# Optimization experiments

Hardware: AMD Instinct MI355X
Metric: run time of the kernel (lower is better)

The kernel has to match this reference:

```python
import jax, jax.numpy as jnp
import numpy as np

B, S, D = 4, 2048, 2048
H = 16
Q_LORA = 1536
KV_LORA = 512
D_NOPE = 128
D_ROPE = 64
D_V = 128
MLP = 8192
EPS = 1e-6
THETA = 10000.0


def rmsnorm(x, scale, eps=EPS):
    var = jnp.mean(jnp.square(x.astype(jnp.float32)), axis=-1, keepdims=True)
    return (x * jax.lax.rsqrt(var + eps)).astype(x.dtype) * scale


def rope(x, positions):
    # x: [B, S, H, d], positions: [B, S]
    d = x.shape[-1]
    inv_freq = 1.0 / (THETA ** (jnp.arange(0, d, 2, dtype=jnp.float32) / d))
    ang = positions.astype(jnp.float32)[..., None] * inv_freq  # [B,S,d/2]
    cos = jnp.cos(ang)[:, :, None, :]
    sin = jnp.sin(ang)[:, :, None, :]
    x1, x2 = jnp.split(x, 2, axis=-1)
    return jnp.concatenate([x1 * cos - x2 * sin, x2 * cos + x1 * sin], axis=-1)


def setup_inputs() -> dict:
    key = jax.random.key(0)
    ks = jax.random.split(key, 16)
    sd = lambda fan: 1.0 / np.sqrt(fan)
    inp = {
        'inputs': jax.random.normal(ks[0], (B, S, D), jnp.float32),
        'decoder_segment_ids': jnp.ones((B, S), jnp.int32),
        'decoder_positions': jnp.broadcast_to(jnp.arange(S, dtype=jnp.int32), (B, S)),
        'pre_ln_scale': jnp.ones((D,), jnp.float32),
        'post_ln_scale': jnp.ones((D,), jnp.float32),
        'q_ln_scale': jnp.ones((Q_LORA,), jnp.float32),
        'kv_ln_scale': jnp.ones((KV_LORA,), jnp.float32),
        'wq_a': jax.random.normal(ks[1], (D, Q_LORA), jnp.float32) * sd(D),
        'wq_b': jax.random.normal(ks[2], (Q_LORA, H, D_NOPE + D_ROPE), jnp.float32) * sd(Q_LORA),
        'wkv_a': jax.random.normal(ks[3], (D, KV_LORA + D_ROPE), jnp.float32) * sd(D),
        'wkv_b': jax.random.normal(ks[4], (KV_LORA, H, D_NOPE + D_V), jnp.float32) * sd(KV_LORA),
        'wo_attn': jax.random.normal(ks[5], (H, D_V, D), jnp.float32) * sd(H * D_V),
        'wi_0': jax.random.normal(ks[6], (D, MLP), jnp.float32) * sd(D),
        'wi_1': jax.random.normal(ks[7], (D, MLP), jnp.float32) * sd(D),
        'wo_mlp': jax.random.normal(ks[8], (MLP, D), jnp.float32) * sd(MLP),
    }
    return inp


def reference(inputs, decoder_segment_ids, decoder_positions, pre_ln_scale, post_ln_scale,
              q_ln_scale, kv_ln_scale, wq_a, wq_b, wkv_a, wkv_b, wo_attn, wi_0, wi_1, wo_mlp):
    # ---- pre-norm ----
    lnx = rmsnorm(inputs, pre_ln_scale)

    # ---- MLA attention ----
    # low-rank query: down-proj, norm, up-proj
    q_c = rmsnorm(lnx @ wq_a, q_ln_scale)                       # [B,S,Q_LORA]
    q = jnp.einsum('bsr,rhd->bshd', q_c, wq_b)                  # [B,S,H,nope+rope]
    q_nope, q_rope = q[..., :D_NOPE], q[..., D_NOPE:]

    # compressed kv + decoupled rope key
    kv = lnx @ wkv_a                                            # [B,S,KV_LORA+rope]
    c_kv = rmsnorm(kv[..., :KV_LORA], kv_ln_scale)
    k_rope = kv[..., KV_LORA:][:, :, None, :]                   # [B,S,1,rope]
    kvu = jnp.einsum('bsr,rhd->bshd', c_kv, wkv_b)              # [B,S,H,nope+v]
    k_nope, v = kvu[..., :D_NOPE], kvu[..., D_NOPE:]

    q_rope = rope(q_rope, decoder_positions)
    k_rope = rope(k_rope, decoder_positions)
    k_rope = jnp.broadcast_to(k_rope, (B, S, H, D_ROPE))

    qf = jnp.concatenate([q_nope, q_rope], axis=-1)             # [B,S,H,192]
    kf = jnp.concatenate([k_nope, k_rope], axis=-1)

    scale = 1.0 / np.sqrt(D_NOPE + D_ROPE)
    scores = jnp.einsum('bqhd,bkhd->bhqk', qf, kf) * scale      # [B,H,S,S]

    pos = decoder_positions
    seg = decoder_segment_ids
    mask = (pos[:, :, None] >= pos[:, None, :]) & (seg[:, :, None] == seg[:, None, :])
    scores = jnp.where(mask[:, None, :, :], scores, -1e9)
    probs = jax.nn.softmax(scores, axis=-1)

    attn = jnp.einsum('bhqk,bkhd->bqhd', probs, v)              # [B,S,H,D_V]
    attn_out = jnp.einsum('bqhd,hdm->bqm', attn, wo_attn)       # [B,S,D]

    # ---- residual + post-norm ----
    intermediate = inputs + attn_out
    hidden = rmsnorm(intermediate, post_ln_scale)

    # ---- gated MLP (silu * linear) ----
    mlp = (jax.nn.silu(hidden @ wi_0) * (hidden @ wi_1)) @ wo_mlp

    return mlp + intermediate
```

## Files before the change

### kernel.cpp

```cpp
#include <hip/hip_runtime.h>
#include <stdint.h>

typedef unsigned short u16;
typedef __bf16 bf16x8 __attribute__((ext_vector_type(8)));
typedef float f32x4 __attribute__((ext_vector_type(4)));

#define B_ 4
#define S_ 2048
#define H_ 16
#define TOK (B_*S_)
#define MFMA_B16 __builtin_amdgcn_mfma_f32_16x16x32_bf16

__device__ __forceinline__ u16 f32_bf16(float f) {
    union { float f; unsigned int u; } x; x.f = f;
    return (u16)((x.u + 0x7fffu + ((x.u >> 16) & 1u)) >> 16);
}
__device__ __forceinline__ float bf2f(u16 v) {
    union { unsigned int u; float f; } x; x.u = ((unsigned int)v) << 16; return x.f;
}
__device__ __forceinline__ void gld_lds16(const u16* g, u16* lds) {
    __builtin_amdgcn_global_load_lds(
        (const __attribute__((address_space(1))) unsigned int*)g,
        (__attribute__((address_space(3))) unsigned int*)lds, 16, 0, 0);
}

__global__ void fill_sentinel(float* o, int n) {
    int i = blockIdx.x * 256 + threadIdx.x;
    if (i < n) o[i] = 12345.0f;
}

__global__ __launch_bounds__(256) void transpose_f32_bf16(const float* __restrict__ in, u16* __restrict__ out,
                                                          int K, int N, int Npad) {
    __shared__ float t[32][33];
    int nb = blockIdx.x * 32, kb = blockIdx.y * 32;
    int c = threadIdx.x & 31, r = threadIdx.x >> 5;
#pragma unroll
    for (int i = 0; i < 4; ++i) {
        int kk = kb + r + i * 8, nn = nb + c;
        t[r + i * 8][c] = (kk < K && nn < N) ? in[(size_t)kk * N + nn] : 0.f;
    }
    __syncthreads();
#pragma unroll
    for (int i = 0; i < 4; ++i) {
        int no = nb + r + i * 8, ko = kb + c;
        if (no < Npad && ko < K) out[(size_t)no * K + ko] = f32_bf16(t[c][r + i * 8]);
    }
}

__global__ __launch_bounds__(256) void rmsnorm_f32(const float* __restrict__ in, const float* __restrict__ sc,
                                                   u16* __restrict__ out, int N) {
    int row = blockIdx.x;
    const float* x = in + (size_t)row * N;
    float ss = 0.f;
    for (int c = threadIdx.x * 4; c < N; c += 1024) {
        float4 v = *(const float4*)(x + c);
        ss += v.x * v.x + v.y * v.y + v.z * v.z + v.w * v.w;
    }
#pragma unroll
    for (int off = 32; off; off >>= 1) ss += __shfl_down(ss, off);
    __shared__ float red[4];
    if ((threadIdx.x & 63) == 0) red[threadIdx.x >> 6] = ss;
    __syncthreads();
    float rs = rsqrtf((red[0] + red[1] + red[2] + red[3]) / (float)N + 1e-6f);
    for (int c = threadIdx.x * 4; c < N; c += 1024) {
        float4 v = *(const float4*)(x + c);
        float4 s4 = *(const float4*)(sc + c);
        ushort4 ov;
        ov.x = f32_bf16(v.x * rs * s4.x);
        ov.y = f32_bf16(v.y * rs * s4.y);
        ov.z = f32_bf16(v.z * rs * s4.z);
        ov.w = f32_bf16(v.w * rs * s4.w);
        *(ushort4*)&out[(size_t)row * N + c] = ov;
    }
}

__global__ __launch_bounds__(256) void rmsnorm_bf16(const u16* __restrict__ in, const float* __restrict__ sc,
                                                    u16* __restrict__ out, int N) {
    int row = blockIdx.x;
    const u16* x = in + (size_t)row * N;
    float ss = 0.f;
    for (int c = threadIdx.x * 8; c < N; c += 2048) {
        ushort4 v0 = *(const ushort4*)(x + c);
        ushort4 v1 = *(const ushort4*)(x + c + 4);
        float f0 = bf2f(v0.x), f1 = bf2f(v0.y), f2 = bf2f(v0.z), f3 = bf2f(v0.w);
        float f4 = bf2f(v1.x), f5 = bf2f(v1.y), f6 = bf2f(v1.z), f7 = bf2f(v1.w);
        ss += f0*f0 + f1*f1 + f2*f2 + f3*f3 + f4*f4 + f5*f5 + f6*f6 + f7*f7;
    }
#pragma unroll
    for (int off = 32; off; off >>= 1) ss += __shfl_down(ss, off);
    __shared__ float red[4];
    if ((threadIdx.x & 63) == 0) red[threadIdx.x >> 6] = ss;
    __syncthreads();
    float rs = rsqrtf((red[0] + red[1] + red[2] + red[3]) / (float)N + 1e-6f);
    for (int c = threadIdx.x * 8; c < N; c += 2048) {
        ushort4 v0 = *(const ushort4*)(x + c);
        ushort4 v1 = *(const ushort4*)(x + c + 4);
        ushort4 o0, o1;
        o0.x = f32_bf16(bf2f(v0.x) * rs * sc[c + 0]);
        o0.y = f32_bf16(bf2f(v0.y) * rs * sc[c + 1]);
        o0.z = f32_bf16(bf2f(v0.z) * rs * sc[c + 2]);
        o0.w = f32_bf16(bf2f(v0.w) * rs * sc[c + 3]);
        o1.x = f32_bf16(bf2f(v1.x) * rs * sc[c + 4]);
        o1.y = f32_bf16(bf2f(v1.y) * rs * sc[c + 5]);
        o1.z = f32_bf16(bf2f(v1.z) * rs * sc[c + 6]);
        o1.w = f32_bf16(bf2f(v1.w) * rs * sc[c + 7]);
        *(ushort4*)&out[(size_t)row * N + c] = o0;
        *(ushort4*)&out[(size_t)row * N + c + 4] = o1;
    }
}

__global__ __launch_bounds__(128) void kv_post(const u16* __restrict__ kv, const float* __restrict__ scale,
                                               const int* __restrict__ pos, u16* __restrict__ ckv,
                                               u16* __restrict__ kr) {
    int row = blockIdx.x;
    const u16* x = kv + (size_t)row * 640;
    int c = threadIdx.x * 4;
    ushort4 v = *(const ushort4*)(x + c);
    float f0 = bf2f(v.x), f1 = bf2f(v.y), f2 = bf2f(v.z), f3 = bf2f(v.w);
    float ss = f0*f0 + f1*f1 + f2*f2 + f3*f3;
#pragma unroll
    for (int off = 32; off; off >>= 1) ss += __shfl_down(ss, off);
    __shared__ float red[2];
    if ((threadIdx.x & 63) == 0) red[threadIdx.x >> 6] = ss;
    __syncthreads();
    float rs = rsqrtf((red[0] + red[1]) * (1.f / 512.f) + 1e-6f);
    float4 s4 = *(const float4*)(scale + c);
    ushort4 ov;
    ov.x = f32_bf16(f0 * rs * s4.x);
    ov.y = f32_bf16(f1 * rs * s4.y);
    ov.z = f32_bf16(f2 * rs * s4.z);
    ov.w = f32_bf16(f3 * rs * s4.w);
    *(ushort4*)&ckv[(size_t)row * 512 + c] = ov;
    if (threadIdx.x < 32) {
        int i = threadIdx.x;
        float x1 = bf2f(x[512 + i]), x2 = bf2f(x[544 + i]);
        float inv = expf(-(float)(2 * i) * (1.f / 64.f) * 9.2103403719761836f);
        float ang = (float)pos[row] * inv;
        float sn, cs; sincosf(ang, &sn, &cs);
        kr[(size_t)row * 64 + i]      = f32_bf16(x1 * cs - x2 * sn);
        kr[(size_t)row * 64 + 32 + i] = f32_bf16(x2 * cs + x1 * sn);
    }
}

__global__ __launch_bounds__(64) void q_rope_inplace(u16* __restrict__ q, const int* __restrict__ pos) {
    int token = blockIdx.x, h = blockIdx.y;
    u16* p = q + ((size_t)token * 16 + h) * 192;
    int t = threadIdx.x, i = t & 31;
    float x1 = bf2f(p[128 + i]), x2 = bf2f(p[160 + i]);
    float inv = expf(-(float)(2 * i) * (1.f / 64.f) * 9.2103403719761836f);
    float ang = (float)pos[token] * inv;
    float sn, cs; sincosf(ang, &sn, &cs);
    float val = (t < 32) ? (x1 * cs - x2 * sn) : (x2 * cs + x1 * sn);
    p[128 + t] = f32_bf16(val);
}

__global__ __launch_bounds__(320) void kv_build(const u16* __restrict__ kvu, const u16* __restrict__ kr,
                                                u16* __restrict__ kf, u16* __restrict__ vf, int tok0) {
    int local = blockIdx.x, h = blockIdx.y;
    int token = tok0 + local;
    int b = token >> 11, s = token & 2047;
    int bh = b * 16 + h;
    int tile = s >> 6, ki = s & 63;
    const u16* u = kvu + ((size_t)local * 16 + h) * 256;
    int t = threadIdx.x;
    if (t < 192) {
        u16 val = (t < 128) ? u[t] : kr[(size_t)token * 64 + (t - 128)];
        int byte = (ki * 384 + t * 2) ^ ((ki & 7) << 4);
        kf[(size_t)bh * (S_ * 192) + (size_t)tile * 12288 + (byte >> 1)] = val;
    } else {
        int dv = t - 192;
        u16 val = u[128 + dv];
        int byte = (dv * 128 + ki * 2) ^ ((dv & 7) << 4);
        vf[(size_t)bh * (S_ * 128) + (size_t)tile * 8192 + (byte >> 1)] = val;
    }
}

__global__ __launch_bounds__(256) void gemm128(const u16* __restrict__ A, const u16* __restrict__ Bt,
                                               u16* __restrict__ C, int M, int N, int K) {
    __shared__ u16 As[128 * 32];
    __shared__ u16 Bs[128 * 32];
    const int l = threadIdx.x & 63, w = threadIdx.x >> 6;
    const int wr = w >> 1, wc = w & 1;
    const int m0 = blockIdx.y * 128, n0 = blockIdx.x * 128;
    const int lm = l & 15, lg = l >> 4;
    const int srow = l >> 2, sk = (l & 3) * 8;
    f32x4 acc[4][4] = {};
    for (int k0 = 0; k0 < K; k0 += 32) {
#pragma unroll
        for (int i = 0; i < 2; ++i) {
            int c = w * 2 + i;
            gld_lds16(A  + (size_t)(m0 + c * 16 + srow) * K + k0 + sk, &As[c * 512]);
            gld_lds16(Bt + (size_t)(n0 + c * 16 + srow) * K + k0 + sk, &Bs[c * 512]);
        }
        __syncthreads();
        bf16x8 a[4], b[4];
#pragma unroll
        for (int m = 0; m < 4; ++m) a[m] = *(const bf16x8*)&As[(wr * 64 + m * 16 + lm) * 32 + lg * 8];
#pragma unroll
        for (int n = 0; n < 4; ++n) b[n] = *(const bf16x8*)&Bs[(wc * 64 + n * 16 + lm) * 32 + lg * 8];
#pragma unroll
        for (int m = 0; m < 4; ++m)
#pragma unroll
            for (int n = 0; n < 4; ++n)
                acc[m][n] = MFMA_B16(a[m], b[n], acc[m][n], 0, 0, 0);
        __syncthreads();
    }
#pragma unroll
    for (int m = 0; m < 4; ++m)
#pragma unroll
        for (int j = 0; j < 4; ++j) {
            int row = m0 + wr * 64 + m * 16 + lg * 4 + j;
            size_t base = (size_t)row * N + n0 + wc * 64;
#pragma unroll
            for (int n = 0; n < 4; ++n)
                C[base + n * 16 + lm] = f32_bf16(acc[m][n][j]);
        }
}

template<int EPI>
__global__ __launch_bounds__(512, 2) void gemm256(const u16* __restrict__ A, const u16* __restrict__ Bt,
                                                  void* __restrict__ Cv, const void* __restrict__ Rv,
                                                  int M, int N, int K) {
    __shared__ u16 lds[65536];
    char* ldsb = (char*)lds;
    const int tid = threadIdx.x;
    const int l = tid & 63, w = tid >> 6;
    const int wr = w >> 2, wcn = w & 3;
    const int lm = l & 15, lg = l >> 4;
    const int m0 = blockIdx.y * 256, n0 = blockIdx.x * 256;

    int gm[2], gk[2];
#pragma unroll
    for (int ld = 0; ld < 2; ++ld) {
        int P = tid * 16 + ld * 8192;
        int row = P >> 7;
        int un = (P & 127) ^ ((row & 7) << 4);
        gm[ld] = row * 2 + (un >> 6);
        gk[ld] = (un & 63) >> 1;
    }
    const u16* Ab = A + (size_t)m0 * K;
    const u16* Bb = Bt + (size_t)n0 * K;

    f32x4 acc[8][4] = {};

    auto stageA = [&](int t) {
#pragma unroll
        for (int ld = 0; ld < 2; ++ld)
            gld_lds16(Ab + (size_t)gm[ld] * K + t * 32 + gk[ld],
                      (u16*)(ldsb + (t & 3) * 32768 + tid * 16 + ld * 8192));
    };
    auto stageB = [&](int t) {
#pragma unroll
        for (int ld = 0; ld < 2; ++ld)
            gld_lds16(Bb + (size_t)gm[ld] * K + t * 32 + gk[ld],
                      (u16*)(ldsb + (t & 3) * 32768 + 16384 + tid * 16 + ld * 8192));
    };
    auto readA = [&](int buf, int fm) -> bf16x8 {
        int m = wr * 128 + fm * 16 + lm;
        int off = ((m & 1) * 64 + lg * 16) ^ (((m >> 1) & 7) << 4);
        return *(const bf16x8*)(ldsb + buf * 32768 + (m >> 1) * 128 + off);
    };
    auto readB = [&](int buf, int fn) -> bf16x8 {
        int n = wcn * 64 + fn * 16 + lm;
        int off = ((n & 1) * 64 + lg * 16) ^ (((n >> 1) & 7) << 4);
        return *(const bf16x8*)(ldsb + buf * 32768 + 16384 + (n >> 1) * 128 + off);
    };

    const int ntile = K >> 5;
    stageA(0); stageB(0);
    stageA(1); stageB(1);
    stageA(2); stageB(2);
    asm volatile("s_waitcnt vmcnt(8)" ::: "memory");
    __builtin_amdgcn_s_barrier();

#pragma unroll 1
    for (int t = 0; t < ntile; ++t) {
        const int buf = t & 3;
        bf16x8 b0 = readB(buf, 0), b1 = readB(buf, 1), b2 = readB(buf, 2), b3 = readB(buf, 3);
        bf16x8 a0 = readA(buf, 0), a1 = readA(buf, 1), a2 = readA(buf, 2), a3 = readA(buf, 3);
        if (t + 3 < ntile) stageA(t + 3);
        asm volatile("s_waitcnt lgkmcnt(0)" ::: "memory");
        __builtin_amdgcn_s_barrier();
        __builtin_amdgcn_sched_barrier(0);
        __builtin_amdgcn_s_setprio(1);
        acc[0][0] = MFMA_B16(a0, b0, acc[0][0], 0, 0, 0);
        acc[0][1] = MFMA_B16(a0, b1, acc[0][1], 0, 0, 0);
        acc[0][2] = MFMA_B16(a0, b2, acc[0][2], 0, 0, 0);
        acc[0][3] = MFMA_B16(a0, b3, acc[0][3], 0, 0, 0);
        acc[1][0] = MFMA_B16(a1, b0, acc[1][0], 0, 0, 0);
        acc[1][1] = MFMA_B16(a1, b1, acc[1][1], 0, 0, 0);
        acc[1][2] = MFMA_B16(a1, b2, acc[1][2], 0, 0, 0);
        acc[1][3] = MFMA_B16(a1, b3, acc[1][3], 0, 0, 0);
        acc[2][0] = MFMA_B16(a2, b0, acc[2][0], 0, 0, 0);
        acc[2][1] = MFMA_B16(a2, b1, acc[2][1], 0, 0, 0);
        acc[2][2] = MFMA_B16(a2, b2, acc[2][2], 0, 0, 0);
        acc[2][3] = MFMA_B16(a2, b3, acc[2][3], 0, 0, 0);
        acc[3][0] = MFMA_B16(a3, b0, acc[3][0], 0, 0, 0);
        acc[3][1] = MFMA_B16(a3, b1, acc[3][1], 0, 0, 0);
        acc[3][2] = MFMA_B16(a3, b2, acc[3][2], 0, 0, 0);
        acc[3][3] = MFMA_B16(a3, b3, acc[3][3], 0, 0, 0);
        __builtin_amdgcn_s_setprio(0);
        __builtin_amdgcn_s_barrier();
        a0 = readA(buf, 4); a1 = readA(buf, 5); a2 = readA(buf, 6); a3 = readA(buf, 7);
        if (t + 3 < ntile) stageB(t + 3);
        asm volatile("s_waitcnt lgkmcnt(0)" ::: "memory");
        if (t < ntile - 3)       { asm volatile("s_waitcnt vmcnt(8)" ::: "memory"); }
        else if (t == ntile - 3) { asm volatile("s_waitcnt vmcnt(4)" ::: "memory"); }
        else if (t == ntile - 2) { asm volatile("s_waitcnt vmcnt(0)" ::: "memory"); }
        __builtin_amdgcn_s_barrier();
        __builtin_amdgcn_sched_barrier(0);
        __builtin_amdgcn_s_setprio(1);
        acc[4][0] = MFMA_B16(a0, b0, acc[4][0], 0, 0, 0);
        acc[4][1] = MFMA_B16(a0, b1, acc[4][1], 0, 0, 0);
        acc[4][2] = MFMA_B16(a0, b2, acc[4][2], 0, 0, 0);
        acc[4][3] = MFMA_B16(a0, b3, acc[4][3], 0, 0, 0);
        acc[5][0] = MFMA_B16(a1, b0, acc[5][0], 0, 0, 0);
        acc[5][1] = MFMA_B16(a1, b1, acc[5][1], 0, 0, 0);
        acc[5][2] = MFMA_B16(a1, b2, acc[5][2], 0, 0, 0);
        acc[5][3] = MFMA_B16(a1, b3, acc[5][3], 0, 0, 0);
        acc[6][0] = MFMA_B16(a2, b0, acc[6][0], 0, 0, 0);
        acc[6][1] = MFMA_B16(a2, b1, acc[6][1], 0, 0, 0);
        acc[6][2] = MFMA_B16(a2, b2, acc[6][2], 0, 0, 0);
        acc[6][3] = MFMA_B16(a2, b3, acc[6][3], 0, 0, 0);
        acc[7][0] = MFMA_B16(a3, b0, acc[7][0], 0, 0, 0);
        acc[7][1] = MFMA_B16(a3, b1, acc[7][1], 0, 0, 0);
        acc[7][2] = MFMA_B16(a3, b2, acc[7][2], 0, 0, 0);
        acc[7][3] = MFMA_B16(a3, b3, acc[7][3], 0, 0, 0);
        __builtin_amdgcn_s_setprio(0);
        __builtin_amdgcn_s_barrier();
    }
#pragma unroll
    for (int fm = 0; fm < 8; ++fm)
#pragma unroll
        for (int j = 0; j < 4; ++j) {
            int row = m0 + wr * 128 + fm * 16 + lg * 4 + j;
            size_t base = (size_t)row * N + n0 + wcn * 64;
#pragma unroll
            for (int fn = 0; fn < 4; ++fn) {
                size_t idx = base + fn * 16 + lm;
                float v = acc[fm][fn][j];
                if (EPI == 0) {
                    ((u16*)Cv)[idx] = f32_bf16(v);
                } else if (EPI == 1) {
                    ((float*)Cv)[idx] = v + ((const float*)Rv)[idx];
                } else {
                    float x0 = bf2f(((const u16*)Rv)[idx]);
                    float sl = x0 / (1.f + expf(-x0));
                    ((u16*)Cv)[idx] = f32_bf16(sl * v);
                }
            }
        }
}

__global__ __launch_bounds__(256) void attn_fwd(const u16* __restrict__ qf, const u16* __restrict__ kfs,
                                                const u16* __restrict__ vfs, u16* __restrict__ attn) {
    __shared__ u16 Ks[64 * 192];
    __shared__ u16 Vs[128 * 64];
    __shared__ u16 Ps[4][1024];
    const int px = blockIdx.x;
    const int bh = blockIdx.y;
    const int b = bh >> 4, h = bh & 15;
    const int l = threadIdx.x & 63, w = threadIdx.x >> 6;
    const int lm = l & 15, g = l >> 4;
    const u16* kb0 = kfs + (size_t)bh * (S_ * 192);
    const u16* vb0 = vfs + (size_t)bh * (S_ * 128);
    const float scale = 0.07216878364870322f;

    for (int pass = 0; pass < 2; ++pass) {
        const int qb = pass ? (31 - px) : px;
        const int qrow = qb * 64 + w * 16 + lm;
        const u16* qp = qf + (((size_t)(b * S_ + qrow)) * 16 + h) * 192 + g * 8;
        bf16x8 qr[6];
#pragma unroll
        for (int c = 0; c < 6; ++c) qr[c] = *(const bf16x8*)(qp + c * 32);
        f32x4 o[8] = {};
        float mrow[4] = {-1e30f, -1e30f, -1e30f, -1e30f};
        float lrow[4] = {0.f, 0.f, 0.f, 0.f};
        for (int kt = 0; kt <= qb; ++kt) {
            const u16* kc = kb0 + (size_t)kt * 12288;
            const u16* vc = vb0 + (size_t)kt * 8192;
#pragma unroll
            for (int i = 0; i < 6; ++i) {
                int c = w + i * 4;
                gld_lds16(kc + c * 512 + l * 8, &Ks[c * 512]);
            }
#pragma unroll
            for (int i = 0; i < 4; ++i) {
                int c = w + i * 4;
                gld_lds16(vc + c * 512 + l * 8, &Vs[c * 512]);
            }
            __syncthreads();
            f32x4 sc[4] = {};
#pragma unroll
            for (int nf = 0; nf < 4; ++nf) {
                int key = nf * 16 + lm;
                int kswz = (key & 7) << 4;
#pragma unroll
                for (int c = 0; c < 6; ++c) {
                    int byte = (key * 384 + (c * 32 + g * 8) * 2) ^ kswz;
                    bf16x8 kv = *(const bf16x8*)((const char*)Ks + byte);
                    sc[nf] = MFMA_B16(qr[c], kv, sc[nf], 0, 0, 0);
                }
            }
#pragma unroll
            for (int j = 0; j < 4; ++j) {
                const int q_g = qb * 64 + w * 16 + g * 4 + j;
                float mx = -1e30f;
#pragma unroll
                for (int nf = 0; nf < 4; ++nf) {
                    int key_g = kt * 64 + nf * 16 + lm;
                    float v = sc[nf][j] * scale;
                    v = (key_g > q_g) ? -1e30f : v;
                    sc[nf][j] = v;
                    mx = fmaxf(mx, v);
                }
                mx = fmaxf(mx, __shfl_xor(mx, 1));
                mx = fmaxf(mx, __shfl_xor(mx, 2));
                mx = fmaxf(mx, __shfl_xor(mx, 4));
                mx = fmaxf(mx, __shfl_xor(mx, 8));
                float newm = fmaxf(mrow[j], mx);
                float fac = __expf(mrow[j] - newm);
                mrow[j] = newm;
                float rs = 0.f;
                u16 pb[4];
#pragma unroll
                for (int nf = 0; nf < 4; ++nf) {
                    float pv = __expf(sc[nf][j] - newm);
                    rs += pv;
                    pb[nf] = f32_bf16(pv);
                }
                rs += __shfl_xor(rs, 1);
                rs += __shfl_xor(rs, 2);
                rs += __shfl_xor(rs, 4);
                rs += __shfl_xor(rs, 8);
                lrow[j] = lrow[j] * fac + rs;
#pragma unroll
                for (int n = 0; n < 8; ++n) o[n][j] *= fac;
                int row = g * 4 + j;
                int rswz = (row & 7) << 4;
#pragma unroll
                for (int nf = 0; nf < 4; ++nf) {
                    int byte = (row * 128 + (nf * 16 + lm) * 2) ^ rswz;
                    *(u16*)((char*)&Ps[w][0] + byte) = pb[nf];
                }
            }
#pragma unroll
            for (int kc2 = 0; kc2 < 2; ++kc2) {
                int pbyte = (lm * 128 + (kc2 * 32 + g * 8) * 2) ^ ((lm & 7) << 4);
                bf16x8 pa = *(const bf16x8*)((const char*)&Ps[w][0] + pbyte);
#pragma unroll
                for (int n = 0; n < 8; ++n) {
                    int dv = n * 16 + lm;
                    int vbyte = (dv * 128 + (kc2 * 32 + g * 8) * 2) ^ ((dv & 7) << 4);
                    bf16x8 vv = *(const bf16x8*)((const char*)Vs + vbyte);
                    o[n] = MFMA_B16(pa, vv, o[n], 0, 0, 0);
                }
            }
            __syncthreads();
        }
#pragma unroll
        for (int j = 0; j < 4; ++j) {
            float inv = 1.f / lrow[j];
            int s = qb * 64 + w * 16 + g * 4 + j;
            size_t base = ((size_t)(b * S_ + s)) * (H_ * 128) + h * 128;
#pragma unroll
            for (int n = 0; n < 8; ++n)
                attn[base + n * 16 + lm] = f32_bf16(o[n][j] * inv);
        }
    }
}

extern "C" void kernel_launch(void* const* d_in, const int* in_sizes, int n_in,
                              void* d_out, int out_size, void* d_ws, size_t ws_size,
                              hipStream_t stream) {
    (void)in_sizes; (void)n_in;
    const float* inputs = (const float*)d_in[0];
    const int*   pos    = (const int*)d_in[2];
    const float* pre_s  = (const float*)d_in[3];
    const float* post_s = (const float*)d_in[4];
    const float* q_s    = (const float*)d_in[5];
    const float* kv_s   = (const float*)d_in[6];
    const float* wq_a   = (const float*)d_in[7];
    const float* wq_b   = (const float*)d_in[8];
    const float* wkv_a  = (const float*)d_in[9];
    const float* wkv_b  = (const float*)d_in[10];
    const float* wo_at  = (const float*)d_in[11];
    const float* wi0    = (const float*)d_in[12];
    const float* wi1    = (const float*)d_in[13];
    const float* wom    = (const float*)d_in[14];
    float* out = (float*)d_out;

    char* p = (char*)d_ws;
    auto alloc = [&](size_t n) { char* r = p; p += (n + 255) & ~(size_t)255; return r; };
    char* R1   = alloc((size_t)134217728);
    u16* vf    = (u16*)alloc((size_t)33554432);
    u16* aslot = (u16*)alloc((size_t)33554432);
    u16* wslot = (u16*)alloc((size_t)33554432);
    u16* ckv   = (u16*)alloc((size_t)8388608);
    u16* krope = (u16*)alloc((size_t)1048576);
    if ((size_t)(p - (char*)d_ws) > ws_size) {
        fill_sentinel<<<(out_size + 255) / 256, 256, 0, stream>>>(out, out_size);
        return;
    }
    u16* kf    = (u16*)R1;
    u16* q_c   = (u16*)R1;
    u16* kvtmp = (u16*)(R1 + 25165824);
    u16* q     = (u16*)(R1 + 50331648);
    u16* lnx   = (u16*)(R1 + 100663296);
    u16* kvu   = (u16*)(R1 + 100663296);
    u16* X     = (u16*)R1;

    rmsnorm_f32<<<TOK, 256, 0, stream>>>(inputs, pre_s, lnx, 2048);
    transpose_f32_bf16<<<dim3(48, 64), 256, 0, stream>>>(wq_a, wslot, 2048, 1536, 1536);
    gemm256<0><<<dim3(6, 32), 512, 0, stream>>>(lnx, wslot, q_c, nullptr, TOK, 1536, 2048);
    rmsnorm_bf16<<<TOK, 256, 0, stream>>>(q_c, q_s, q_c, 1536);
    transpose_f32_bf16<<<dim3(20, 64), 256, 0, stream>>>(wkv_a, wslot, 2048, 576, 640);
    gemm128<<<dim3(5, 64), 256, 0, stream>>>(lnx, wslot, kvtmp, TOK, 640, 2048);
    kv_post<<<TOK, 128, 0, stream>>>(kvtmp, kv_s, pos, ckv, krope);
    transpose_f32_bf16<<<dim3(96, 48), 256, 0, stream>>>(wq_b, wslot, 1536, 3072, 3072);
    gemm256<0><<<dim3(12, 32), 512, 0, stream>>>(q_c, wslot, q, nullptr, TOK, 3072, 1536);
    q_rope_inplace<<<dim3(TOK, 16), 64, 0, stream>>>(q, pos);
    transpose_f32_bf16<<<dim3(128, 16), 256, 0, stream>>>(wkv_b, wslot, 512, 4096, 4096);
    for (int ch = 0; ch < 2; ++ch) {
        int t0 = ch * 4096;
        gemm256<0><<<dim3(16, 16), 512, 0, stream>>>(ckv + (size_t)t0 * 512, wslot, kvu, nullptr, 4096, 4096, 512);
        kv_build<<<dim3(4096, 16), 320, 0, stream>>>(kvu, krope, kf, vf, t0);
    }
    attn_fwd<<<dim3(16, 64), 256, 0, stream>>>(q, kf, vf, aslot);
    transpose_f32_bf16<<<dim3(64, 64), 256, 0, stream>>>(wo_at, wslot, 2048, 2048, 2048);
    gemm256<1><<<dim3(8, 32), 512, 0, stream>>>(aslot, wslot, out, inputs, TOK, 2048, 2048);
    rmsnorm_f32<<<TOK, 256, 0, stream>>>(out, post_s, aslot, 2048);
    transpose_f32_bf16<<<dim3(256, 64), 256, 0, stream>>>(wi0, wslot, 2048, 8192, 8192);
    gemm256<0><<<dim3(32, 32), 512, 0, stream>>>(aslot, wslot, X, nullptr, TOK, 8192, 2048);
    transpose_f32_bf16<<<dim3(256, 64), 256, 0, stream>>>(wi1, wslot, 2048, 8192, 8192);
    gemm256<2><<<dim3(32, 32), 512, 0, stream>>>(aslot, wslot, X, X, TOK, 8192, 2048);
    transpose_f32_bf16<<<dim3(64, 256), 256, 0, stream>>>(wom, wslot, 8192, 2048, 2048);
    gemm256<1><<<dim3(8, 32), 512, 0, stream>>>(X, wslot, out, out, TOK, 2048, 8192);
}
```

Baseline: 1.736 ms.

## Restructure GEMM to 64-wide K tiles with XCD swizzle; pipeline K/V loads in attention

The 256x256 GEMM moves from four 32-wide K buffers to two 64-wide double buffers with a new LDS layout and a reordered four-phase MFMA schedule. Launch bounds drop to one block per CU, and block IDs are remapped so neighbouring tiles land on the same XCD for better L2 reuse. The attention kernel also remaps blocks per XCD and splits K and V staging, prefetching the next K tile while softmax runs, to overlap global loads with compute. The risks are lower occupancy in the GEMM and a shallower prefetch depth, which may expose memory latency.

```diff
diff --git a/kernel.cpp b/kernel.cpp
--- a/kernel.cpp
+++ b/kernel.cpp
@@ -10,6 +10,8 @@
 #define H_ 16
 #define TOK (B_*S_)
 #define MFMA_B16 __builtin_amdgcn_mfma_f32_16x16x32_bf16
+#define LGKM0 asm volatile("s_waitcnt lgkmcnt(0)" ::: "memory")
+#define VMC(n) asm volatile("s_waitcnt vmcnt(" #n ")" ::: "memory")
 
 __device__ __forceinline__ u16 f32_bf16(float f) {
     union { float f; unsigned int u; } x; x.f = f;
@@ -218,7 +220,7 @@
 }
 
 template<int EPI>
-__global__ __launch_bounds__(512, 2) void gemm256(const u16* __restrict__ A, const u16* __restrict__ Bt,
+__global__ __launch_bounds__(512, 1) void gemm256(const u16* __restrict__ A, const u16* __restrict__ Bt,
                                                   void* __restrict__ Cv, const void* __restrict__ Rv,
                                                   int M, int N, int K) {
     __shared__ u16 lds[65536];
@@ -227,105 +229,148 @@
     const int l = tid & 63, w = tid >> 6;
     const int wr = w >> 2, wcn = w & 3;
     const int lm = l & 15, lg = l >> 4;
-    const int m0 = blockIdx.y * 256, n0 = blockIdx.x * 256;
-
-    int gm[2], gk[2];
+
+    const int gx = gridDim.x;
+    const int nwg = gx * gridDim.y;
+    const int lin = blockIdx.y * gx + blockIdx.x;
+    const int swz = (lin & 7) * (nwg >> 3) + (lin >> 3);
+    const int m0 = (swz / gx) * 256, n0 = (swz % gx) * 256;
+
+    int sr[2], sc[2];
 #pragma unroll
     for (int ld = 0; ld < 2; ++ld) {
         int P = tid * 16 + ld * 8192;
-        int row = P >> 7;
-        int un = (P & 127) ^ ((row & 7) << 4);
-        gm[ld] = row * 2 + (un >> 6);
-        gk[ld] = (un & 63) >> 1;
+        sr[ld] = P >> 7;
+        sc[ld] = (P & 127) ^ ((sr[ld] & 7) << 4);
     }
     const u16* Ab = A + (size_t)m0 * K;
     const u16* Bb = Bt + (size_t)n0 * K;
 
     f32x4 acc[8][4] = {};
 
-    auto stageA = [&](int t) {
+    auto stage = [&](const u16* gp, int mb, int h, int t) {
 #pragma unroll
         for (int ld = 0; ld < 2; ++ld)
-            gld_lds16(Ab + (size_t)gm[ld] * K + t * 32 + gk[ld],
-                      (u16*)(ldsb + (t & 3) * 32768 + tid * 16 + ld * 8192));
+            gld_lds16(gp + (size_t)(h * 128 + sr[ld]) * K + t * 64 + (sc[ld] >> 1),
+                      (u16*)(ldsb + (t & 1) * 65536 + mb + h * 16384 + tid * 16 + ld * 8192));
     };
-    auto stageB = [&](int t) {
-#pragma unroll
-        for (int ld = 0; ld < 2; ++ld)
-            gld_lds16(Bb + (size_t)gm[ld] * K + t * 32 + gk[ld],
-                      (u16*)(ldsb + (t & 3) * 32768 + 16384 + tid * 16 + ld * 8192));
+    auto readA = [&](int buf, int fm, int ks) -> bf16x8 {
+        int m = wr * 128 + fm * 16 + lm;
+        int r = m & 127;
+        int byte = (ks * 64 + lg * 16) ^ ((r & 7) << 4);
+        return *(const bf16x8*)(ldsb + buf * 65536 + (m >> 7) * 16384 + r * 128 + byte);
     };
-    auto readA = [&](int buf, int fm) -> bf16x8 {
-        int m = wr * 128 + fm * 16 + lm;
-        int off = ((m & 1) * 64 + lg * 16) ^ (((m >> 1) & 7) << 4);
-        return *(const bf16x8*)(ldsb + buf * 32768 + (m >> 1) * 128 + off);
+    auto readB = [&](int buf, int fn, int ks) -> bf16x8 {
+        int n = wcn * 64 + fn * 16 + lm;
+        int r = n & 127;
+        int byte = (ks * 64 + lg * 16) ^ ((r & 7) << 4);
+        return *(const bf16x8*)(ldsb + buf * 65536 + 32768 + (n >> 7) * 16384 + r * 128 + byte);
     };
-    auto readB = [&](int buf, int fn) -> bf16x8 {
-        int n = wcn * 64 + fn * 16 + lm;
-        int off = ((n & 1) * 64 + lg * 16) ^ (((n >> 1) & 7) << 4);
-        return *(const bf16x8*)(ldsb + buf * 32768 + 16384 + (n >> 1) * 128 + off);
-    };
-
-    const int ntile = K >> 5;
-    stageA(0); stageB(0);
-    stageA(1); stageB(1);
-    stageA(2); stageB(2);
-    asm volatile("s_waitcnt vmcnt(8)" ::: "memory");
+
+    const int nt = K >> 6;
+    stage(Ab, 0, 0, 0); stage(Ab, 0, 1, 0);
+    stage(Bb, 32768, 0, 0); stage(Bb, 32768, 1, 0);
+    VMC(0);
     __builtin_amdgcn_s_barrier();
 
 #pragma unroll 1
-    for (int t = 0; t < ntile; ++t) {
-        const int buf = t & 3;
-        bf16x8 b0 = readB(buf, 0), b1 = readB(buf, 1), b2 = readB(buf, 2), b3 = readB(buf, 3);
-        bf16x8 a0 = readA(buf, 0), a1 = readA(buf, 1), a2 = readA(buf, 2), a3 = readA(buf, 3);
-        if (t + 3 < ntile) stageA(t + 3);
-        asm volatile("s_waitcnt lgkmcnt(0)" ::: "memory");
-        __builtin_amdgcn_s_barrier();
+    for (int t = 0; t < nt; ++t) {
+        const int buf = t & 1;
+        const bool nx = (t + 1 < nt);
+        bf16x8 a0, a1, a2, a3, a4, a5, a6, a7;
+        bf16x8 b0 = readB(buf, 0, 0), b1 = readB(buf, 0, 1), b2 = readB(buf, 1, 0), b3 = readB(buf, 1, 1);
+        a0 = readA(buf, 0, 0); a1 = readA(buf, 0, 1); a2 = readA(buf, 1, 0); a3 = readA(buf, 1, 1);
+        a4 = readA(buf, 2, 0); a5 = readA(buf, 2, 1); a6 = readA(buf, 3, 0); a7 = readA(buf, 3, 1);
+        if (nx) { stage(Ab, 0, 0, t + 1); stage(Ab, 0, 1, t + 1); }
+        __builtin_amdgcn_s_barrier();
+        LGKM0;
         __builtin_amdgcn_sched_barrier(0);
         __builtin_amdgcn_s_setprio(1);
         acc[0][0] = MFMA_B16(a0, b0, acc[0][0], 0, 0, 0);
-        acc[0][1] = MFMA_B16(a0, b1, acc[0][1], 0, 0, 0);
-        acc[0][2] = MFMA_B16(a0, b2, acc[0][2], 0, 0, 0);
-        acc[0][3] = MFMA_B16(a0, b3, acc[0][3], 0, 0, 0);
-        acc[1][0] = MFMA_B16(a1, b0, acc[1][0], 0, 0, 0);
-        acc[1][1] = MFMA_B16(a1, b1, acc[1][1], 0, 0, 0);
-        acc[1][2] = MFMA_B16(a1, b2, acc[1][2], 0, 0, 0);
-        acc[1][3] = MFMA_B16(a1, b3, acc[1][3], 0, 0, 0);
-        acc[2][0] = MFMA_B16(a2, b0, acc[2][0], 0, 0, 0);
-        acc[2][1] = MFMA_B16(a2, b1, acc[2][1], 0, 0, 0);
-        acc[2][2] = MFMA_B16(a2, b2, acc[2][2], 0, 0, 0);
-        acc[2][3] = MFMA_B16(a2, b3, acc[2][3], 0, 0, 0);
-        acc[3][0] = MFMA_B16(a3, b0, acc[3][0], 0, 0, 0);
-        acc[3][1] = MFMA_B16(a3, b1, acc[3][1], 0, 0, 0);
-        acc[3][2] = MFMA_B16(a3, b2, acc[3][2], 0, 0, 0);
-        acc[3][3] = MFMA_B16(a3, b3, acc[3][3], 0, 0, 0);
+        acc[0][0] = MFMA_B16(a1, b1, acc[0][0], 0, 0, 0);
+        acc[0][1] = MFMA_B16(a0, b2, acc[0][1], 0, 0, 0);
+        acc[0][1] = MFMA_B16(a1, b3, acc[0][1], 0, 0, 0);
+        acc[1][0] = MFMA_B16(a2, b0, acc[1][0], 0, 0, 0);
+        acc[1][0] = MFMA_B16(a3, b1, acc[1][0], 0, 0, 0);
+        acc[1][1] = MFMA_B16(a2, b2, acc[1][1], 0, 0, 0);
+        acc[1][1] = MFMA_B16(a3, b3, acc[1][1], 0, 0, 0);
+        acc[2][0] = MFMA_B16(a4, b0, acc[2][0], 0, 0, 0);
+        acc[2][0] = MFMA_B16(a5, b1, acc[2][0], 0, 0, 0);
+        acc[2][1] = MFMA_B16(a4, b2, acc[2][1], 0, 0, 0);
+        acc[2][1] = MFMA_B16(a5, b3, acc[2][1], 0, 0, 0);
+        acc[3][0] = MFMA_B16(a6, b0, acc[3][0], 0, 0, 0);
+        acc[3][0] = MFMA_B16(a7, b1, acc[3][0], 0, 0, 0);
+        acc[3][1] = MFMA_B16(a6, b2, acc[3][1], 0, 0, 0);
+        acc[3][1] = MFMA_B16(a7, b3, acc[3][1], 0, 0, 0);
         __builtin_amdgcn_s_setprio(0);
         __builtin_amdgcn_s_barrier();
-        a0 = readA(buf, 4); a1 = readA(buf, 5); a2 = readA(buf, 6); a3 = readA(buf, 7);
-        if (t + 3 < ntile) stageB(t + 3);
-        asm volatile("s_waitcnt lgkmcnt(0)" ::: "memory");
-        if (t < ntile - 3)       { asm volatile("s_waitcnt vmcnt(8)" ::: "memory"); }
-        else if (t == ntile - 3) { asm volatile("s_waitcnt vmcnt(4)" ::: "memory"); }
-        else if (t == ntile - 2) { asm volatile("s_waitcnt vmcnt(0)" ::: "memory"); }
-        __builtin_amdgcn_s_barrier();
+        bf16x8 c0 = readB(buf, 2, 0), c1 = readB(buf, 2, 1), c2 = readB(buf, 3, 0), c3 = readB(buf, 3, 1);
+        if (nx) { stage(Bb, 32768, 0, t + 1); stage(Bb, 32768, 1, t + 1); }
+        __builtin_amdgcn_s_barrier();
+        LGKM0;
         __builtin_amdgcn_sched_barrier(0);
         __builtin_amdgcn_s_setprio(1);
+        acc[0][2] = MFMA_B16(a0, c0, acc[0][2], 0, 0, 0);
+        acc[0][2] = MFMA_B16(a1, c1, acc[0][2], 0, 0, 0);
+        acc[0][3] = MFMA_B16(a0, c2, acc[0][3], 0, 0, 0);
+        acc[0][3] = MFMA_B16(a1, c3, acc[0][3], 0, 0, 0);
+        acc[1][2] = MFMA_B16(a2, c0, acc[1][2], 0, 0, 0);
+        acc[1][2] = MFMA_B16(a3, c1, acc[1][2], 0, 0, 0);
+        acc[1][3] = MFMA_B16(a2, c2, acc[1][3], 0, 0, 0);
+        acc[1][3] = MFMA_B16(a3, c3, acc[1][3], 0, 0, 0);
+        acc[2][2] = MFMA_B16(a4, c0, acc[2][2], 0, 0, 0);
+        acc[2][2] = MFMA_B16(a5, c1, acc[2][2], 0, 0, 0);
+        acc[2][3] = MFMA_B16(a4, c2, acc[2][3], 0, 0, 0);
+        acc[2][3] = MFMA_B16(a5, c3, acc[2][3], 0, 0, 0);
+        acc[3][2] = MFMA_B16(a6, c0, acc[3][2], 0, 0, 0);
+        acc[3][2] = MFMA_B16(a7, c1, acc[3][2], 0, 0, 0);
+        acc[3][3] = MFMA_B16(a6, c2, acc[3][3], 0, 0, 0);
+        acc[3][3] = MFMA_B16(a7, c3, acc[3][3], 0, 0, 0);
+        __builtin_amdgcn_s_setprio(0);
+        __builtin_amdgcn_s_barrier();
+        a0 = readA(buf, 4, 0); a1 = readA(buf, 4, 1); a2 = readA(buf, 5, 0); a3 = readA(buf, 5, 1);
+        a4 = readA(buf, 6, 0); a5 = readA(buf, 6, 1); a6 = readA(buf, 7, 0); a7 = readA(buf, 7, 1);
+        __builtin_amdgcn_s_barrier();
+        LGKM0;
+        __builtin_amdgcn_sched_barrier(0);
+        __builtin_amdgcn_s_setprio(1);
+        acc[4][2] = MFMA_B16(a0, c0, acc[4][2], 0, 0, 0);
+        acc[4][2] = MFMA_B16(a1, c1, acc[4][2], 0, 0, 0);
+        acc[4][3] = MFMA_B16(a0, c2, acc[4][3], 0, 0, 0);
+        acc[4][3] = MFMA_B16(a1, c3, acc[4][3], 0, 0, 0);
+        acc[5][2] = MFMA_B16(a2, c0, acc[5][2], 0, 0, 0);
+        acc[5][2] = MFMA_B16(a3, c1, acc[5][2], 0, 0, 0);
+        acc[5][3] = MFMA_B16(a2, c2, acc[5][3], 0, 0, 0);
+        acc[5][3] = MFMA_B16(a3, c3, acc[5][3], 0, 0, 0);
+        acc[6][2] = MFMA_B16(a4, c0, acc[6][2], 0, 0, 0);
+        acc[6][2] = MFMA_B16(a5, c1, acc[6][2], 0, 0, 0);
+        acc[6][3] = MFMA_B16(a4, c2, acc[6][3], 0, 0, 0);
+        acc[6][3] = MFMA_B16(a5, c3, acc[6][3], 0, 0, 0);
+        acc[7][2] = MFMA_B16(a6, c0, acc[7][2], 0, 0, 0);
+        acc[7][2] = MFMA_B16(a7, c1, acc[7][2], 0, 0, 0);
+        acc[7][3] = MFMA_B16(a6, c2, acc[7][3], 0, 0, 0);
+        acc[7][3] = MFMA_B16(a7, c3, acc[7][3], 0, 0, 0);
+        __builtin_amdgcn_s_setprio(0);
+        __builtin_amdgcn_s_barrier();
+        VMC(0);
+        __builtin_amdgcn_s_barrier();
+        __builtin_amdgcn_s_setprio(1);
         acc[4][0] = MFMA_B16(a0, b0, acc[4][0], 0, 0, 0);
-        acc[4][1] = MFMA_B16(a0, b1, acc[4][1], 0, 0, 0);
-        acc[4][2] = MFMA_B16(a0, b2, acc[4][2], 0, 0, 0);
-        acc[4][3] = MFMA_B16(a0, b3, acc[4][3], 0, 0, 0);
-        acc[5][0] = MFMA_B16(a1, b0, acc[5][0], 0, 0, 0);
-        acc[5][1] = MFMA_B16(a1, b1, acc[5][1], 0, 0, 0);
-        acc[5][2] = MFMA_B16(a1, b2, acc[5][2], 0, 0, 0);
-        acc[5][3] = MFMA_B16(a1, b3, acc[5][3], 0, 0, 0);
-        acc[6][0] = MFMA_B16(a2, b0, acc[6][0], 0, 0, 0);
-        acc[6][1] = MFMA_B16(a2, b1, acc[6][1], 0, 0, 0);
-        acc[6][2] = MFMA_B16(a2, b2, acc[6][2], 0, 0, 0);
-        acc[6][3] = MFMA_B16(a2, b3, acc[6][3], 0, 0, 0);
-        acc[7][0] = MFMA_B16(a3, b0, acc[7][0], 0, 0, 0);
-        acc[7][1] = MFMA_B16(a3, b1, acc[7][1], 0, 0, 0);
-        acc[7][2] = MFMA_B16(a3, b2, acc[7][2], 0, 0, 0);
-        acc[7][3] = MFMA_B16(a3, b3, acc[7][3], 0, 0, 0);
+        acc[4][0] = MFMA_B16(a1, b1, acc[4][0], 0, 0, 0);
+        acc[4][1] = MFMA_B16(a0, b2, acc[4][1], 0, 0, 0);
+        acc[4][1] = MFMA_B16(a1, b3, acc[4][1], 0, 0, 0);
+        acc[5][0] = MFMA_B16(a2, b0, acc[5][0], 0, 0, 0);
+        acc[5][0] = MFMA_B16(a3, b1, acc[5][0], 0, 0, 0);
+        acc[5][1] = MFMA_B16(a2, b2, acc[5][1], 0, 0, 0);
+        acc[5][1] = MFMA_B16(a3, b3, acc[5][1], 0, 0, 0);
+        acc[6][0] = MFMA_B16(a4, b0, acc[6][0], 0, 0, 0);
+        acc[6][0] = MFMA_B16(a5, b1, acc[6][0], 0, 0, 0);
+        acc[6][1] = MFMA_B16(a4, b2, acc[6][1], 0, 0, 0);
+        acc[6][1] = MFMA_B16(a5, b3, acc[6][1], 0, 0, 0);
+        acc[7][0] = MFMA_B16(a6, b0, acc[7][0], 0, 0, 0);
+        acc[7][0] = MFMA_B16(a7, b1, acc[7][0], 0, 0, 0);
+        acc[7][1] = MFMA_B16(a6, b2, acc[7][1], 0, 0, 0);
+        acc[7][1] = MFMA_B16(a7, b3, acc[7][1], 0, 0, 0);
         __builtin_amdgcn_s_setprio(0);
         __builtin_amdgcn_s_barrier();
     }
@@ -352,13 +397,15 @@
         }
 }
 
-__global__ __launch_bounds__(256) void attn_fwd(const u16* __restrict__ qf, const u16* __restrict__ kfs,
-                                                const u16* __restrict__ vfs, u16* __restrict__ attn) {
+__global__ __launch_bounds__(256, 3) void attn_fwd(const u16* __restrict__ qf, const u16* __restrict__ kfs,
+                                                   const u16* __restrict__ vfs, u16* __restrict__ attn) {
     __shared__ u16 Ks[64 * 192];
     __shared__ u16 Vs[128 * 64];
     __shared__ u16 Ps[4][1024];
-    const int px = blockIdx.x;
-    const int bh = blockIdx.y;
+    const int lin = blockIdx.y * gridDim.x + blockIdx.x;
+    const int xcd = lin & 7, j = lin >> 3;
+    const int bh = xcd * 8 + (j >> 4);
+    const int px = j & 15;
     const int b = bh >> 4, h = bh & 15;
     const int l = threadIdx.x & 63, w = threadIdx.x >> 6;
     const int lm = l & 15, g = l >> 4;
@@ -366,6 +413,25 @@
     const u16* vb0 = vfs + (size_t)bh * (S_ * 128);
     const float scale = 0.07216878364870322f;
 
+    auto stageK = [&](int kt2) {
+        const u16* kc = kb0 + (size_t)kt2 * 12288;
+#pragma unroll
+        for (int i = 0; i < 6; ++i) {
+            int c = w + i * 4;
+            gld_lds16(kc + c * 512 + l * 8, &Ks[c * 512]);
+        }
+    };
+    auto stageV = [&](int kt2) {
+        const u16* vc = vb0 + (size_t)kt2 * 8192;
+#pragma unroll
+        for (int i = 0; i < 4; ++i) {
+            int c = w + i * 4;
+            gld_lds16(vc + c * 512 + l * 8, &Vs[c * 512]);
+        }
+    };
+
+    stageK(0);
+
     for (int pass = 0; pass < 2; ++pass) {
         const int qb = pass ? (31 - px) : px;
         const int qrow = qb * 64 + w * 16 + lm;
@@ -377,19 +443,8 @@
         float mrow[4] = {-1e30f, -1e30f, -1e30f, -1e30f};
         float lrow[4] = {0.f, 0.f, 0.f, 0.f};
         for (int kt = 0; kt <= qb; ++kt) {
-            const u16* kc = kb0 + (size_t)kt * 12288;
-            const u16* vc = vb0 + (size_t)kt * 8192;
-#pragma unroll
-            for (int i = 0; i < 6; ++i) {
-                int c = w + i * 4;
-                gld_lds16(kc + c * 512 + l * 8, &Ks[c * 512]);
-            }
-#pragma unroll
-            for (int i = 0; i < 4; ++i) {
-                int c = w + i * 4;
-                gld_lds16(vc + c * 512 + l * 8, &Vs[c * 512]);
-            }
             __syncthreads();
+            stageV(kt);
             f32x4 sc[4] = {};
 #pragma unroll
             for (int nf = 0; nf < 4; ++nf) {
@@ -402,30 +457,33 @@
                     sc[nf] = MFMA_B16(qr[c], kv, sc[nf], 0, 0, 0);
                 }
             }
-#pragma unroll
-            for (int j = 0; j < 4; ++j) {
-                const int q_g = qb * 64 + w * 16 + g * 4 + j;
+            LGKM0;
+            __builtin_amdgcn_s_barrier();
+            if (kt < qb) stageK(kt + 1);
+#pragma unroll
+            for (int jj = 0; jj < 4; ++jj) {
+                const int q_g = qb * 64 + w * 16 + g * 4 + jj;
                 float mx = -1e30f;
 #pragma unroll
                 for (int nf = 0; nf < 4; ++nf) {
                     int key_g = kt * 64 + nf * 16 + lm;
-                    float v = sc[nf][j] * scale;
+                    float v = sc[nf][jj] * scale;
                     v = (key_g > q_g) ? -1e30f : v;
-                    sc[nf][j] = v;
+                    sc[nf][jj] = v;
                     mx = fmaxf(mx, v);
                 }
                 mx = fmaxf(mx, __shfl_xor(mx, 1));
                 mx = fmaxf(mx, __shfl_xor(mx, 2));
                 mx = fmaxf(mx, __shfl_xor(mx, 4));
                 mx = fmaxf(mx, __shfl_xor(mx, 8));
-                float newm = fmaxf(mrow[j], mx);
-                float fac = __expf(mrow[j] - newm);
-                mrow[j] = newm;
+                float newm = fmaxf(mrow[jj], mx);
+                float fac = __expf(mrow[jj] - newm);
+                mrow[jj] = newm;
                 float rs = 0.f;
                 u16 pb[4];
 #pragma unroll
                 for (int nf = 0; nf < 4; ++nf) {
-                    float pv = __expf(sc[nf][j] - newm);
+                    float pv = __expf(sc[nf][jj] - newm);
                     rs += pv;
                     pb[nf] = f32_bf16(pv);
                 }
@@ -433,10 +491,10 @@
                 rs += __shfl_xor(rs, 2);
                 rs += __shfl_xor(rs, 4);
                 rs += __shfl_xor(rs, 8);
-                lrow[j] = lrow[j] * fac + rs;
-#pragma unroll
-                for (int n = 0; n < 8; ++n) o[n][j] *= fac;
-                int row = g * 4 + j;
+                lrow[jj] = lrow[jj] * fac + rs;
+#pragma unroll
+                for (int n = 0; n < 8; ++n) o[n][jj] *= fac;
+                int row = g * 4 + jj;
                 int rswz = (row & 7) << 4;
 #pragma unroll
                 for (int nf = 0; nf < 4; ++nf) {
@@ -444,6 +502,9 @@
                     *(u16*)((char*)&Ps[w][0] + byte) = pb[nf];
                 }
             }
+            if (kt < qb) { VMC(6); } else { VMC(0); }
+            __builtin_amdgcn_s_barrier();
+            __builtin_amdgcn_sched_barrier(0);
 #pragma unroll
             for (int kc2 = 0; kc2 < 2; ++kc2) {
                 int pbyte = (lm * 128 + (kc2 * 32 + g * 8) * 2) ^ ((lm & 7) << 4);
@@ -456,17 +517,17 @@
                     o[n] = MFMA_B16(pa, vv, o[n], 0, 0, 0);
                 }
             }
-            __syncthreads();
         }
 #pragma unroll
-        for (int j = 0; j < 4; ++j) {
-            float inv = 1.f / lrow[j];
-            int s = qb * 64 + w * 16 + g * 4 + j;
+        for (int jj = 0; jj < 4; ++jj) {
+            float inv = 1.f / lrow[jj];
+            int s = qb * 64 + w * 16 + g * 4 + jj;
             size_t base = ((size_t)(b * S_ + s)) * (H_ * 128) + h * 128;
 #pragma unroll
             for (int n = 0; n < 8; ++n)
-                attn[base + n * 16 + lm] = f32_bf16(o[n][j] * inv);
+                attn[base + n * 16 + lm] = f32_bf16(o[n][jj] * inv);
         }
+        if (pass == 0) stageK(0);
     }
 }
 
```

New measurement: 1.666 ms. 1.04x faster.
